# Optimization experiments

Hardware: AMD Instinct MI355X
Metric: run time of the kernel (lower is better)

## Reference

```python
import jax, jax.numpy as jnp
import numpy as np

NX, NY, NZ = 512, 512, 1
C_BEV = 128
C_BEFORE = C_BEV // NZ  # features per z-slice
B = 4
P_PER_BATCH = 80000


def setup_inputs() -> dict:
    key = jax.random.key(0)
    P = B * P_PER_BATCH
    pillar_features = jax.random.normal(key, (P, C_BEFORE), dtype=jnp.float32)
    # Build coords with unique spatial cells per batch so scatter order is irrelevant.
    rng = np.random.default_rng(0)
    cells = NZ * NY * NX
    coords_np = np.empty((P, 4), dtype=np.int32)
    for b in range(B):  # loop over tiny fixed batch count, setup only
        flat = rng.choice(cells, size=P_PER_BATCH, replace=False)
        z = flat // (NY * NX)
        y = (flat // NX) % NY
        x = flat % NX
        s = slice(b * P_PER_BATCH, (b + 1) * P_PER_BATCH)
        coords_np[s, 0] = b
        coords_np[s, 1] = z
        coords_np[s, 2] = y
        coords_np[s, 3] = x
    return {
        "batch_size": B,
        "pillar_features": pillar_features,
        "coords": jnp.asarray(coords_np),
    }


def reference(batch_size, pillar_features, coords):
    # Fused single-pass scatter: global flat index = b*(nz*ny*nx) + z*ny*nx + y*nx + x
    cells = NZ * NY * NX
    flat = (coords[:, 0].astype(jnp.int32) * cells
            + coords[:, 1].astype(jnp.int32) * (NY * NX)
            + coords[:, 2].astype(jnp.int32) * NX
            + coords[:, 3].astype(jnp.int32))
    canvas = jnp.zeros((batch_size * cells, C_BEFORE), dtype=pillar_features.dtype)
    canvas = canvas.at[flat].set(pillar_features)
    # [B*nz*ny*nx, C] -> [B, nz, ny, nx, C] -> [B, C, nz, ny, nx] -> [B, C*nz, ny, nx]
    canvas = canvas.reshape(batch_size, NZ, NY, NX, C_BEFORE)
    canvas = jnp.transpose(canvas, (0, 4, 1, 2, 3))
    return canvas.reshape(batch_size, C_BEFORE * NZ, NY, NX)
```

## Files before the change

kernel.cpp:

```cpp
#include <hip/hip_runtime.h>


#define NXD 512
#define NYD 512
#define NZD 1
#define CB  128
#define CELLS (NXD * NYD * NZD)

__global__ void k_init_map(int* __restrict__ map, int n4) {
    int i = blockIdx.x * blockDim.x + threadIdx.x;
    if (i < n4) ((int4*)map)[i] = make_int4(-1, -1, -1, -1);
}

__global__ void k_scatter_idx(const int* __restrict__ coords,
                              int* __restrict__ map, int P) {
    int p = blockIdx.x * blockDim.x + threadIdx.x;
    if (p >= P) return;
    int4 c = ((const int4*)coords)[p];
    int cell = c.y * (NYD * NXD) + c.z * NXD + c.w;
    map[c.x * CELLS + cell] = p;
}

__global__ __launch_bounds__(256) void k_gather(const float* __restrict__ feat,
                                                const int* __restrict__ map,
                                                float* __restrict__ out) {
    __shared__ int   pidx[64];
    __shared__ float tile[64][CB + 1];

    const int t = threadIdx.x;
    const int tiles_per_b = CELLS / 64;
    const int b = blockIdx.x / tiles_per_b;
    const int cell_base = (blockIdx.x % tiles_per_b) * 64;

    if (t < 64) pidx[t] = map[b * CELLS + cell_base + t];
    __syncthreads();

    {
        const int c4 = t & 31;
        const int r0 = t >> 5;
        #pragma unroll
        for (int rr = 0; rr < 8; ++rr) {
            const int x = rr * 8 + r0;
            const int idx = pidx[x];
            float4 v = make_float4(0.f, 0.f, 0.f, 0.f);
            if (idx >= 0) v = ((const float4*)feat)[(size_t)idx * (CB / 4) + c4];
            tile[x][c4 * 4 + 0] = v.x;
            tile[x][c4 * 4 + 1] = v.y;
            tile[x][c4 * 4 + 2] = v.z;
            tile[x][c4 * 4 + 3] = v.w;
        }
    }
    __syncthreads();

    {
        const int x4 = t & 15;
        const int cr = t >> 4;
        float* outb = out + (size_t)b * CB * CELLS + cell_base + x4 * 4;
        #pragma unroll
        for (int cc = 0; cc < 8; ++cc) {
            const int c = cc * 16 + cr;
            float4 v;
            v.x = tile[x4 * 4 + 0][c];
            v.y = tile[x4 * 4 + 1][c];
            v.z = tile[x4 * 4 + 2][c];
            v.w = tile[x4 * 4 + 3][c];
            *reinterpret_cast<float4*>(outb + (size_t)c * CELLS) = v;
        }
    }
}

extern "C" void kernel_launch(void* const* d_in, const int* in_sizes, int n_in,
                              void* d_out, int out_size, void* d_ws, size_t ws_size,
                              hipStream_t stream) {
    const float* feat   = (const float*)d_in[1];
    const int*   coords = (const int*)d_in[2];
    float*       out    = (float*)d_out;
    int*         map    = (int*)d_ws;

    const int B = out_size / (CB * CELLS);
    const int P = in_sizes[1] / CB;
    const int n_map = B * CELLS;

    k_init_map<<<(n_map / 4 + 255) / 256, 256, 0, stream>>>(map, n_map / 4);
    k_scatter_idx<<<(P + 255) / 256, 256, 0, stream>>>(coords, map, P);
    k_gather<<<B * (CELLS / 64), 256, 0, stream>>>(feat, map, out);
}
```

Before: 186.7 us.

## Double gather tile size, use nontemporal loads/stores, memset the index map

The gather kernel now handles 128 cells per block instead of 64. It preloads all pillar indices into registers before issuing the feature loads, and uses nontemporal loads and stores to keep streaming output and feature traffic out of the caches. The custom map-init kernel is replaced by hipMemsetAsync with 0xFF, which gives -1 for every int. The larger tile roughly doubles LDS use per block, which may lower occupancy, in exchange for wider 512-byte contiguous output rows per channel.

```diff
diff --git a/kernel.cpp b/kernel.cpp
--- a/kernel.cpp
+++ b/kernel.cpp
@@ -7,10 +7,9 @@
 #define CB  128
 #define CELLS (NXD * NYD * NZD)
 
-__global__ void k_init_map(int* __restrict__ map, int n4) {
-    int i = blockIdx.x * blockDim.x + threadIdx.x;
-    if (i < n4) ((int4*)map)[i] = make_int4(-1, -1, -1, -1);
-}
+#define TILE 128
+
+typedef float f4 __attribute__((ext_vector_type(4)));
 
 __global__ void k_scatter_idx(const int* __restrict__ coords,
                               int* __restrict__ map, int P) {
@@ -24,26 +23,30 @@
 __global__ __launch_bounds__(256) void k_gather(const float* __restrict__ feat,
                                                 const int* __restrict__ map,
                                                 float* __restrict__ out) {
-    __shared__ int   pidx[64];
-    __shared__ float tile[64][CB + 1];
+    __shared__ int   pidx[TILE];
+    __shared__ float tile[TILE][CB + 1];
 
     const int t = threadIdx.x;
-    const int tiles_per_b = CELLS / 64;
+    const int tiles_per_b = CELLS / TILE;
     const int b = blockIdx.x / tiles_per_b;
-    const int cell_base = (blockIdx.x % tiles_per_b) * 64;
+    const int cell_base = (blockIdx.x % tiles_per_b) * TILE;
 
-    if (t < 64) pidx[t] = map[b * CELLS + cell_base + t];
+    if (t < TILE) pidx[t] = map[b * CELLS + cell_base + t];
     __syncthreads();
 
     {
         const int c4 = t & 31;
         const int r0 = t >> 5;
+        int idxr[16];
         #pragma unroll
-        for (int rr = 0; rr < 8; ++rr) {
+        for (int rr = 0; rr < 16; ++rr) idxr[rr] = pidx[rr * 8 + r0];
+        #pragma unroll
+        for (int rr = 0; rr < 16; ++rr) {
             const int x = rr * 8 + r0;
-            const int idx = pidx[x];
-            float4 v = make_float4(0.f, 0.f, 0.f, 0.f);
-            if (idx >= 0) v = ((const float4*)feat)[(size_t)idx * (CB / 4) + c4];
+            f4 v = (f4)(0.f);
+            if (idxr[rr] >= 0)
+                v = __builtin_nontemporal_load(
+                        (const f4*)feat + (size_t)idxr[rr] * (CB / 4) + c4);
             tile[x][c4 * 4 + 0] = v.x;
             tile[x][c4 * 4 + 1] = v.y;
             tile[x][c4 * 4 + 2] = v.z;
@@ -53,18 +56,19 @@
     __syncthreads();
 
     {
-        const int x4 = t & 15;
-        const int cr = t >> 4;
-        float* outb = out + (size_t)b * CB * CELLS + cell_base + x4 * 4;
+        const int x4 = t & 31;
+        const int cr = t >> 5;
+        float* outb = out + (size_t)b * CB * CELLS + cell_base;
         #pragma unroll
-        for (int cc = 0; cc < 8; ++cc) {
-            const int c = cc * 16 + cr;
-            float4 v;
+        for (int cc = 0; cc < 16; ++cc) {
+            const int c = cc * 8 + cr;
+            f4 v;
             v.x = tile[x4 * 4 + 0][c];
             v.y = tile[x4 * 4 + 1][c];
             v.z = tile[x4 * 4 + 2][c];
             v.w = tile[x4 * 4 + 3][c];
-            *reinterpret_cast<float4*>(outb + (size_t)c * CELLS) = v;
+            __builtin_nontemporal_store(
+                v, (f4*)(outb + (size_t)c * CELLS + x4 * 4));
         }
     }
 }
@@ -81,7 +85,7 @@
     const int P = in_sizes[1] / CB;
     const int n_map = B * CELLS;
 
-    k_init_map<<<(n_map / 4 + 255) / 256, 256, 0, stream>>>(map, n_map / 4);
+    (void)hipMemsetAsync(map, 0xFF, (size_t)n_map * sizeof(int), stream);
     k_scatter_idx<<<(P + 255) / 256, 256, 0, stream>>>(coords, map, P);
-    k_gather<<<B * (CELLS / 64), 256, 0, stream>>>(feat, map, out);
+    k_gather<<<B * (CELLS / TILE), 256, 0, stream>>>(feat, map, out);
 }
```

Result: slower. 231.2 us (+23.8%).
